# Kernel tuning notes

Measured on AMD Instinct MI355X. Metric: run time of the kernel, lower is better.

The kernel has to match this reference:

```python
import jax, jax.numpy as jnp
import numpy as np

BS = 8            # self.b from __init__
NSAMPLE = 32      # self.nsample
EPS_TCR = 0.2     # TotalCodingRate eps
COS_EPS = 1e-8    # torch cosine_similarity eps


def setup_inputs() -> dict:
    key = jax.random.key(0)
    k0, k1, k2, k3, k4 = jax.random.split(key, 5)
    B, N, C = 8, 8192, 64
    return {
        "logits": jax.random.normal(k0, (B, N, C), jnp.float32),
        "logits1": jax.random.normal(k1, (B, N, C), jnp.float32),
        "p0first": jax.random.uniform(k2, (B, N, 3), jnp.float32),
        "p0sec": jax.random.uniform(k3, (B, N, 3), jnp.float32),
        "orixyz": jax.random.uniform(k4, (B, N, 3), jnp.float32),
    }


def _fps(p, m):
    # furthest point sampling, seed = point 0; p: [b,n,3] -> idx [b,m] int32
    b, n, _ = p.shape
    batch = jnp.arange(b)
    d0 = jnp.sum((p - p[:, :1]) ** 2, -1)  # [b,n] sq dist to seed

    def step(dist, _):
        nxt = jnp.argmax(dist, axis=1)                 # [b]
        pn = p[batch, nxt]                             # [b,3]
        dist = jnp.minimum(dist, jnp.sum((p - pn[:, None]) ** 2, -1))
        return dist, nxt

    _, idxs = jax.lax.scan(step, d0, None, length=m - 1)  # [m-1,b]
    return jnp.concatenate(
        [jnp.zeros((b, 1), jnp.int32), idxs.T.astype(jnp.int32)], axis=1)


def _knn_idx(q, s, k):
    # q: [b,m,3] queries, s: [b,n,3] support -> [b,m,k] neighbor indices
    d = (jnp.sum(q * q, -1)[:, :, None] + jnp.sum(s * s, -1)[:, None, :]
         - 2.0 * jnp.einsum('bmd,bnd->bmn', q, s))
    _, idx = jax.lax.top_k(-d, k)  # smallest distances
    return idx


def _group_losses(fi, fj, c):
    # fi: [b,m,c] center feats, fj: [b,m,k,c] neighbor feats
    # per group: datatemp = cat(fj, fi) -> [K=k+1, c]
    D = jnp.concatenate([fj, fi[:, :, None, :]], axis=2)  # [b,m,K,c]
    avg = D.mean(axis=2, keepdims=True)                   # [b,m,1,c]
    num = jnp.sum(D * avg, -1)                            # [b,m,K]
    den = jnp.maximum(
        jnp.linalg.norm(D, axis=-1) * jnp.linalg.norm(avg, axis=-1), COS_EPS)
    loss_contract = -(num / den).mean(axis=2)             # [b,m] (Similarity_Loss)
    # TotalCodingRate on each single row z: -0.5*logdet(I + (c/(BS*eps)) z z^T)
    #   = -0.5*log(1 + (c/(BS*eps)) ||z||^2)   (rank-1 identity)
    scalar = c / (BS * EPS_TCR)
    loss_tcr = (-0.5 * jnp.log1p(scalar * jnp.sum(D * D, -1))).mean(axis=2)
    return jnp.sum(200.0 * loss_contract + 1.0 * loss_tcr, axis=1)  # [b]


def reference(logits, logits1, p0first, p0sec, orixyz):
    b, n, c = logits.shape
    ds = n // 16  # downsample

    # global per-point cosine loss
    num = jnp.sum(logits * logits1, -1)
    den = jnp.maximum(
        jnp.linalg.norm(logits, axis=-1) * jnp.linalg.norm(logits1, axis=-1),
        COS_EPS)
    globalpointloss = -jnp.mean(num / den)

    idx = _fps(p0first, ds)   # [b,ds]
    idx1 = _fps(p0sec, ds)
    new_p = jnp.take_along_axis(p0first, idx[..., None], axis=1)   # [b,ds,3]
    new_p1 = jnp.take_along_axis(p0sec, idx1[..., None], axis=1)
    fi = jnp.take_along_axis(logits, idx[..., None], axis=1)       # [b,ds,c]
    fi1 = jnp.take_along_axis(logits1, idx1[..., None], axis=1)

    ki = _knn_idx(new_p, p0first, NSAMPLE)    # [b,ds,k]
    ki1 = _knn_idx(new_p1, p0sec, NSAMPLE)
    fj = jax.vmap(lambda f, i: f[i])(logits, ki)    # [b,ds,k,c]
    fj1 = jax.vmap(lambda f, i: f[i])(logits1, ki1)

    # per-batch summed group-inner losses (both views)
    S = _group_losses(fi, fj, c) + _group_losses(fi1, fj1, c)  # [b]

    # faithful to original: running total divided by downsample each batch iter
    def fold(g, s):
        return (g + s) / ds, None
    groupinnerloss, _ = jax.lax.scan(fold, jnp.float32(0.0), S)
    groupinnerloss = groupinnerloss / b

    # original returns globalpointloss + groupinnerloss + groupinnerloss
    # (groupouterloss is computed but never used in the returned loss)
    return globalpointloss + groupinnerloss + groupinnerloss
```

## Files before the change

kernel.cpp:

```cpp
#include <hip/hip_runtime.h>
#include <cstdint>

#define NPTS 8192
#define NB 8
#define DS 512
#define CF 64
#define KNN 32
#define NFPS 16
#define NWORK 240
#define NCOSI 64
#define NITEMS (NCOSI + 2 * NB * DS)
#define DYNLDS 98304

typedef float v2f __attribute__((ext_vector_type(2)));
typedef unsigned long long ull;

__device__ __forceinline__ float wave_max63(float x) {
  int v;
  v = __builtin_amdgcn_update_dpp(0, __float_as_int(x), 0x111, 0xf, 0xf, true); x = fmaxf(x, __int_as_float(v));
  v = __builtin_amdgcn_update_dpp(0, __float_as_int(x), 0x112, 0xf, 0xf, true); x = fmaxf(x, __int_as_float(v));
  v = __builtin_amdgcn_update_dpp(0, __float_as_int(x), 0x114, 0xf, 0xf, true); x = fmaxf(x, __int_as_float(v));
  v = __builtin_amdgcn_update_dpp(0, __float_as_int(x), 0x118, 0xf, 0xf, true); x = fmaxf(x, __int_as_float(v));
  v = __builtin_amdgcn_update_dpp(0, __float_as_int(x), 0x142, 0xf, 0xf, true); x = fmaxf(x, __int_as_float(v));
  v = __builtin_amdgcn_update_dpp(0, __float_as_int(x), 0x143, 0xf, 0xf, true); x = fmaxf(x, __int_as_float(v));
  return x;
}

__device__ __forceinline__ float wave_sum_bcast(float x) {
  int v;
  v = __builtin_amdgcn_update_dpp(0, __float_as_int(x), 0x111, 0xf, 0xf, true); x += __int_as_float(v);
  v = __builtin_amdgcn_update_dpp(0, __float_as_int(x), 0x112, 0xf, 0xf, true); x += __int_as_float(v);
  v = __builtin_amdgcn_update_dpp(0, __float_as_int(x), 0x114, 0xf, 0xf, true); x += __int_as_float(v);
  v = __builtin_amdgcn_update_dpp(0, __float_as_int(x), 0x118, 0xf, 0xf, true); x += __int_as_float(v);
  v = __builtin_amdgcn_update_dpp(0, __float_as_int(x), 0x142, 0xf, 0xf, true); x += __int_as_float(v);
  v = __builtin_amdgcn_update_dpp(0, __float_as_int(x), 0x143, 0xf, 0xf, true); x += __int_as_float(v);
  return __int_as_float(__builtin_amdgcn_readlane(__float_as_int(x), 63));
}

__global__ __launch_bounds__(64) void zero_kernel(float* __restrict__ acc) {
  if (threadIdx.x < 16) acc[threadIdx.x] = 0.0f;
}

__global__ __launch_bounds__(512, 2) void fused_kernel(
    const float* __restrict__ logits, const float* __restrict__ logits1,
    const float* __restrict__ p0first, const float* __restrict__ p0sec,
    int* __restrict__ idxbuf, float* __restrict__ acc,
    int* __restrict__ done, float* __restrict__ out) {
  extern __shared__ char smem[];
  __shared__ __align__(16) ull wslot[2][8];
  __shared__ int wtot[8];
  __shared__ int s_bl[2];
  __shared__ int ctr, eqctr, s_center;
  __shared__ float wloss[8];

  const int blk = blockIdx.x;
  const int t = threadIdx.x;

  if (blk < NFPS) {
    float* ldsP = (float*)smem;
    const int view = blk >> 3, b = blk & 7;
    const float* p = (view ? p0sec : p0first) + (size_t)b * NPTS * 3;
    int* idx_out = idxbuf + blk * DS;
    const int lane = t & 63, wave = t >> 6;
    v2f px2[8], py2[8], pz2[8], dist2[8];
    {
      float f48[48];
      const float4* p4 = (const float4*)p;
      float4* l4 = (float4*)ldsP;
#pragma unroll
      for (int i = 0; i < 12; ++i) {
        float4 v4 = p4[t * 12 + i];
        l4[t * 12 + i] = v4;
        f48[i * 4 + 0] = v4.x; f48[i * 4 + 1] = v4.y;
        f48[i * 4 + 2] = v4.z; f48[i * 4 + 3] = v4.w;
      }
#pragma unroll
      for (int g = 0; g < 8; ++g) {
        px2[g] = (v2f){f48[6 * g + 0], f48[6 * g + 3]};
        py2[g] = (v2f){f48[6 * g + 1], f48[6 * g + 4]};
        pz2[g] = (v2f){f48[6 * g + 2], f48[6 * g + 5]};
        dist2[g] = (v2f){3.4e38f, 3.4e38f};
      }
    }
#pragma unroll
    for (int g = 0; g < 8; ++g) {
      asm("" : "+v"(px2[g]), "+v"(py2[g]), "+v"(pz2[g]));
    }
    if (t == 0)
      __hip_atomic_store(&idx_out[0], 0, __ATOMIC_RELAXED, __HIP_MEMORY_SCOPE_AGENT);
    float wx = p[0], wy = p[1], wz = p[2];
    __syncthreads();

    for (int it = 0; it < DS - 1; ++it) {
      v2f wx2 = (v2f){wx, wx}, wy2 = (v2f){wy, wy}, wz2 = (v2f){wz, wz};
#pragma unroll
      for (int g = 0; g < 8; ++g) {
        v2f dx = px2[g] - wx2, dy = py2[g] - wy2, dz = pz2[g] - wz2;
        v2f nd = dx * dx + dy * dy + dz * dz;
        dist2[g] = __builtin_elementwise_min(dist2[g], nd);
      }
      v2f m0 = __builtin_elementwise_max(dist2[0], dist2[1]);
      v2f m1 = __builtin_elementwise_max(dist2[2], dist2[3]);
      v2f m2 = __builtin_elementwise_max(dist2[4], dist2[5]);
      v2f m3 = __builtin_elementwise_max(dist2[6], dist2[7]);
      v2f n0 = __builtin_elementwise_max(m0, m1);
      v2f n1 = __builtin_elementwise_max(m2, m3);
      v2f q = __builtin_elementwise_max(n0, n1);
      float lm = fmaxf(q.x, q.y);
      float wmv = wave_max63(lm);
      float wm = __int_as_float(__builtin_amdgcn_readlane(__float_as_int(wmv), 63));
      ull cmask = __ballot(lm == wm);
      int winlane = (int)__ffsll(cmask) - 1;
      if (lane == winlane) {
        int jbest = 0;
#pragma unroll
        for (int jp = 15; jp >= 0; --jp) {
          float dv = (jp & 1) ? dist2[jp >> 1].y : dist2[jp >> 1].x;
          if (dv == lm) jbest = jp;
        }
        unsigned e_best = ((unsigned)t << 4) | (unsigned)jbest;
        wslot[it & 1][wave] =
            (((ull)__float_as_uint(wm)) << 32) | (ull)(8191u - e_best);
      }
      asm volatile("s_waitcnt lgkmcnt(0)\n\ts_barrier" ::: "memory");
      {
        const ull* ws = wslot[it & 1];
        ull k0 = ws[0], k1 = ws[1], k2 = ws[2], k3 = ws[3];
        ull k4 = ws[4], k5 = ws[5], k6 = ws[6], k7 = ws[7];
        ull a0 = k0 > k1 ? k0 : k1, a1 = k2 > k3 ? k2 : k3;
        ull a2 = k4 > k5 ? k4 : k5, a3 = k6 > k7 ? k6 : k7;
        ull b0 = a0 > a1 ? a0 : a1, b1 = a2 > a3 ? a2 : a3;
        ull kb = b0 > b1 ? b0 : b1;
        unsigned e = 8191u - (unsigned)(kb & 0xffffffffu);
        if (t == 0)
          __hip_atomic_store(&idx_out[it + 1], (int)e, __ATOMIC_RELAXED,
                             __HIP_MEMORY_SCOPE_AGENT);
        wx = ldsP[e * 3 + 0]; wy = ldsP[e * 3 + 1]; wz = ldsP[e * 3 + 2];
      }
    }
  } else {
    int* hb0 = (int*)smem;
    int* hb1 = (int*)(smem + 16384);
    float* Drows = (float*)(smem + 32768);
    int* nbr = (int*)(smem + 41216);
    int* eq = (int*)(smem + 41344);
    const int lane = t & 63, wave = t >> 6;
    const int w0 = blk - NFPS;
    for (int item = w0; item < NITEMS; item += NWORK) {
      if (item < NCOSI) {
        float cv = 0.0f;
#pragma unroll
        for (int rr = 0; rr < 2; ++rr) {
          int row = item * 1024 + rr * 512 + t;
          const float4* A = (const float4*)(logits + (size_t)row * CF);
          const float4* Bv = (const float4*)(logits1 + (size_t)row * CF);
          float ab = 0.f, aa = 0.f, bb = 0.f;
#pragma unroll
          for (int i = 0; i < 16; ++i) {
            float4 a = A[i], c4 = Bv[i];
            ab += a.x * c4.x + a.y * c4.y + a.z * c4.z + a.w * c4.w;
            aa += a.x * a.x + a.y * a.y + a.z * a.z + a.w * a.w;
            bb += c4.x * c4.x + c4.y * c4.y + c4.z * c4.z + c4.w * c4.w;
          }
          cv += ab / fmaxf(sqrtf(aa) * sqrtf(bb), 1e-8f);
        }
        cv = wave_sum_bcast(cv);
        if (lane == 0) wloss[wave] = cv;
        __syncthreads();
        if (t == 0) {
          float s = 0.f;
#pragma unroll
          for (int w = 0; w < 8; ++w) s += wloss[w];
          atomicAdd(&acc[0], s);
        }
        __syncthreads();
      } else {
        const int qi2 = item - NCOSI;
        const int m = qi2 >> 4, pair = qi2 & 15;
        const int g = pair * DS + m;
        const int view = pair >> 3, b = pair & 7;
        const float* p = (view ? p0sec : p0first) + (size_t)b * NPTS * 3;
        float f48[48];
        {
          const float4* p4 = (const float4*)p;
#pragma unroll
          for (int i = 0; i < 12; ++i) {
            float4 v4 = p4[t * 12 + i];
            f48[i * 4 + 0] = v4.x; f48[i * 4 + 1] = v4.y;
            f48[i * 4 + 2] = v4.z; f48[i * 4 + 3] = v4.w;
          }
        }
        for (int k = t; k < 4096; k += 512) hb0[k] = 0;
        if (t == 0) {
          int ce;
          while ((unsigned)(ce = __hip_atomic_load(&idxbuf[g], __ATOMIC_RELAXED,
                                                   __HIP_MEMORY_SCOPE_AGENT)) >= 8192u)
            __builtin_amdgcn_s_sleep(2);
          s_center = ce;
        }
        __syncthreads();
        const int ci = s_center;
        const float qx = p[ci * 3], qy = p[ci * 3 + 1], qz = p[ci * 3 + 2];
        const float qq = qx * qx + qy * qy + qz * qz;
        const int cpy = (t & 1) << 11;
        unsigned sk[16];
#pragma unroll
        for (int j = 0; j < 16; ++j) {
          float sx = f48[j * 3], sy = f48[j * 3 + 1], sz = f48[j * 3 + 2];
          float ss = sx * sx + sy * sy + sz * sz;
          float dt = qx * sx + qy * sy + qz * sz;
          float d = qq + ss - 2.0f * dt;
          unsigned u = __float_as_uint(d);
          u = (u & 0x80000000u) ? ~u : (u | 0x80000000u);
          sk[j] = u;
        }
        int rrank = 31;
#pragma unroll
        for (int j = 0; j < 16; ++j) atomicAdd(&hb0[cpy + (sk[j] >> 21)], 1);
        __syncthreads();
        unsigned pA, pAB, V;
        {
          int b0 = t << 2;
          int c0 = hb0[b0] + hb0[2048 + b0];
          int c1 = hb0[b0 + 1] + hb0[2048 + b0 + 1];
          int c2 = hb0[b0 + 2] + hb0[2048 + b0 + 2];
          int c3 = hb0[b0 + 3] + hb0[2048 + b0 + 3];
          int s = c0 + c1 + c2 + c3;
          int inc = s;
#pragma unroll
          for (int o = 1; o < 64; o <<= 1) {
            int v = __shfl_up(inc, o, 64);
            if (lane >= o) inc += v;
          }
          if (lane == 63) wtot[wave] = inc;
          for (int k = t; k < 4096; k += 512) hb1[k] = 0;
          __syncthreads();
          int off = 0;
#pragma unroll
          for (int w = 0; w < 8; ++w) off += (w < wave) ? wtot[w] : 0;
          int exc = off + inc - s;
          if (rrank >= exc && rrank < exc + s) {
            int r2 = rrank - exc; int bin, less;
            if (r2 < c0) { bin = 0; less = 0; }
            else if (r2 < c0 + c1) { bin = 1; less = c0; }
            else if (r2 < c0 + c1 + c2) { bin = 2; less = c0 + c1; }
            else { bin = 3; less = c0 + c1 + c2; }
            s_bl[0] = b0 + bin; s_bl[1] = exc + less;
          }
          __syncthreads();
          pA = (unsigned)s_bl[0];
          rrank -= s_bl[1];
        }
#pragma unroll
        for (int j = 0; j < 16; ++j) {
          unsigned u = sk[j];
          if ((u >> 21) == pA) atomicAdd(&hb1[cpy + ((u >> 10) & 2047)], 1);
        }
        __syncthreads();
        {
          int b0 = t << 2;
          int c0 = hb1[b0] + hb1[2048 + b0];
          int c1 = hb1[b0 + 1] + hb1[2048 + b0 + 1];
          int c2 = hb1[b0 + 2] + hb1[2048 + b0 + 2];
          int c3 = hb1[b0 + 3] + hb1[2048 + b0 + 3];
          int s = c0 + c1 + c2 + c3;
          int inc = s;
#pragma unroll
          for (int o = 1; o < 64; o <<= 1) {
            int v = __shfl_up(inc, o, 64);
            if (lane >= o) inc += v;
          }
          if (lane == 63) wtot[wave] = inc;
          for (int k = t; k < 4096; k += 512) hb0[k] = 0;
          __syncthreads();
          int off = 0;
#pragma unroll
          for (int w = 0; w < 8; ++w) off += (w < wave) ? wtot[w] : 0;
          int exc = off + inc - s;
          if (rrank >= exc && rrank < exc + s) {
            int r2 = rrank - exc; int bin, less;
            if (r2 < c0) { bin = 0; less = 0; }
            else if (r2 < c0 + c1) { bin = 1; less = c0; }
            else if (r2 < c0 + c1 + c2) { bin = 2; less = c0 + c1; }
            else { bin = 3; less = c0 + c1 + c2; }
            s_bl[0] = b0 + bin; s_bl[1] = exc + less;
          }
          __syncthreads();
          pAB = (pA << 11) | (unsigned)s_bl[0];
          rrank -= s_bl[1];
        }
        const int cpyC = (t & 1) << 10;
#pragma unroll
        for (int j = 0; j < 16; ++j) {
          unsigned u = sk[j];
          if ((u >> 10) == pAB) atomicAdd(&hb0[cpyC + (u & 1023)], 1);
        }
        __syncthreads();
        {
          int b0 = t << 1;
          int c0 = hb0[b0] + hb0[1024 + b0];
          int c1 = hb0[b0 + 1] + hb0[1024 + b0 + 1];
          int s = c0 + c1;
          int inc = s;
#pragma unroll
          for (int o = 1; o < 64; o <<= 1) {
            int v = __shfl_up(inc, o, 64);
            if (lane >= o) inc += v;
          }
          if (lane == 63) wtot[wave] = inc;
          __syncthreads();
          int off = 0;
#pragma unroll
          for (int w = 0; w < 8; ++w) off += (w < wave) ? wtot[w] : 0;
          int exc = off + inc - s;
          if (rrank >= exc && rrank < exc + s) {
            int r2 = rrank - exc;
            if (r2 < c0) { s_bl[0] = b0; s_bl[1] = exc; }
            else { s_bl[0] = b0 + 1; s_bl[1] = exc + c0; }
          }
          if (t == 0) { ctr = 0; eqctr = 0; }
          __syncthreads();
          V = (pAB << 10) | (unsigned)s_bl[0];
          rrank -= s_bl[1];
        }
#pragma unroll
        for (int j = 0; j < 16; ++j) {
          unsigned u = sk[j];
          if (u < V) {
            int s = atomicAdd(&ctr, 1);
            nbr[s] = t * 16 + j;
          } else if (u == V) {
            int s2 = atomicAdd(&eqctr, 1);
            if (s2 < 256) eq[s2] = t * 16 + j;
          }
        }
        __syncthreads();
        if (t == 0) {
          int need = rrank + 1;
          int E = eqctr; if (E > 256) E = 256;
          int base = KNN - need;
          for (int s = 0; s < need; ++s) {
            int mi = 0;
            for (int i = 1; i < E; ++i)
              if (eq[i] < eq[mi]) mi = i;
            nbr[base + s] = eq[mi];
            eq[mi] = 0x7fffffff;
          }
        }
        __syncthreads();
        const float* f = (view ? logits1 : logits) + (size_t)b * NPTS * CF;
        for (int r = wave; r < 33; r += 8) {
          int e = (r < 32) ? nbr[r] : ci;
          Drows[r * 64 + lane] = f[(size_t)e * CF + lane];
        }
        __syncthreads();
        float avg = 0.0f;
#pragma unroll
        for (int r = 0; r < 33; ++r) avg += Drows[r * 64 + lane];
        avg *= (1.0f / 33.0f);
        float na = wave_sum_bcast(avg * avg);
        const float rsna = sqrtf(na);
        float loss = 0.0f;
        for (int r = wave; r < 33; r += 8) {
          float d = Drows[r * 64 + lane];
          float d0 = wave_sum_bcast(d * avg);
          float n0 = wave_sum_bcast(d * d);
          float den = fmaxf(sqrtf(n0) * rsna, 1e-8f);
          loss += -200.0f * (d0 / den) - 0.5f * log1pf(40.0f * n0);
        }
        if (lane == 0) wloss[wave] = loss;
        __syncthreads();
        if (t == 0) {
          float s = 0.f;
#pragma unroll
          for (int w = 0; w < 8; ++w) s += wloss[w];
          atomicAdd(&acc[1 + b], s * (1.0f / 33.0f));
        }
        __syncthreads();
      }
    }
    __syncthreads();
    if (t == 0) {
      int d = __hip_atomic_fetch_add(done, 1, __ATOMIC_ACQ_REL, __HIP_MEMORY_SCOPE_AGENT);
      if (d == NWORK - 1) {
        float a0 = __hip_atomic_load(&acc[0], __ATOMIC_ACQUIRE, __HIP_MEMORY_SCOPE_AGENT);
        float gsum = 0.0f;
        for (int bb = 0; bb < 8; ++bb) {
          float Sb = __hip_atomic_load(&acc[1 + bb], __ATOMIC_ACQUIRE, __HIP_MEMORY_SCOPE_AGENT);
          gsum = (gsum + Sb) * (1.0f / 512.0f);
        }
        gsum *= 0.125f;
        out[0] = -a0 / 65536.0f + gsum + gsum;
      }
    }
  }
}

extern "C" void kernel_launch(void* const* d_in, const int* in_sizes, int n_in,
                              void* d_out, int out_size, void* d_ws, size_t ws_size,
                              hipStream_t stream) {
  (void)in_sizes; (void)n_in; (void)out_size; (void)ws_size;
  const float* logits  = (const float*)d_in[0];
  const float* logits1 = (const float*)d_in[1];
  const float* p0first = (const float*)d_in[2];
  const float* p0sec   = (const float*)d_in[3];
  float* out = (float*)d_out;

  float* acc = (float*)d_ws;
  int* done  = (int*)d_ws + 13;
  int* idxbuf = (int*)d_ws + 16;

  zero_kernel<<<1, 64, 0, stream>>>(acc);
  fused_kernel<<<NFPS + NWORK, 512, DYNLDS, stream>>>(logits, logits1, p0first, p0sec,
                                                      idxbuf, acc, done, out);
}
```

Before: 524.6 us.

## Run two FPS instances per block to interleave independent reduction chains

Each FPS block now processes two point clouds at once, so there are 8 FPS blocks instead of 16 and more blocks go to the worker pool. The two independent distance-update and wave-max chains are interleaved to hide DPP and barrier latency and to halve the number of barriers per pair of clouds. The winner's coordinates are now fetched from global memory (L1/L2) instead of an LDS copy, which adds global-load latency on the serial critical path of every iteration. Register pressure also doubles in the FPS path.

```diff
diff --git a/kernel.cpp b/kernel.cpp
--- a/kernel.cpp
+++ b/kernel.cpp
@@ -6,8 +6,8 @@
 #define DS 512
 #define CF 64
 #define KNN 32
-#define NFPS 16
-#define NWORK 240
+#define NFPS 8
+#define NWORK 248
 #define NCOSI 64
 #define NITEMS (NCOSI + 2 * NB * DS)
 #define DYNLDS 98304
@@ -15,15 +15,14 @@
 typedef float v2f __attribute__((ext_vector_type(2)));
 typedef unsigned long long ull;
 
-__device__ __forceinline__ float wave_max63(float x) {
-  int v;
-  v = __builtin_amdgcn_update_dpp(0, __float_as_int(x), 0x111, 0xf, 0xf, true); x = fmaxf(x, __int_as_float(v));
-  v = __builtin_amdgcn_update_dpp(0, __float_as_int(x), 0x112, 0xf, 0xf, true); x = fmaxf(x, __int_as_float(v));
-  v = __builtin_amdgcn_update_dpp(0, __float_as_int(x), 0x114, 0xf, 0xf, true); x = fmaxf(x, __int_as_float(v));
-  v = __builtin_amdgcn_update_dpp(0, __float_as_int(x), 0x118, 0xf, 0xf, true); x = fmaxf(x, __int_as_float(v));
-  v = __builtin_amdgcn_update_dpp(0, __float_as_int(x), 0x142, 0xf, 0xf, true); x = fmaxf(x, __int_as_float(v));
-  v = __builtin_amdgcn_update_dpp(0, __float_as_int(x), 0x143, 0xf, 0xf, true); x = fmaxf(x, __int_as_float(v));
-  return x;
+__device__ __forceinline__ void wave_max63_dual(float& a, float& b) {
+  int va, vb;
+#define DSTEP(ctrl)                                                            \
+  va = __builtin_amdgcn_update_dpp(0, __float_as_int(a), ctrl, 0xf, 0xf, true);\
+  vb = __builtin_amdgcn_update_dpp(0, __float_as_int(b), ctrl, 0xf, 0xf, true);\
+  a = fmaxf(a, __int_as_float(va)); b = fmaxf(b, __int_as_float(vb));
+  DSTEP(0x111) DSTEP(0x112) DSTEP(0x114) DSTEP(0x118) DSTEP(0x142) DSTEP(0x143)
+#undef DSTEP
 }
 
 __device__ __forceinline__ float wave_sum_bcast(float x) {
@@ -47,7 +46,8 @@
     int* __restrict__ idxbuf, float* __restrict__ acc,
     int* __restrict__ done, float* __restrict__ out) {
   extern __shared__ char smem[];
-  __shared__ __align__(16) ull wslot[2][8];
+  __shared__ __align__(16) ull wslotA[2][8];
+  __shared__ __align__(16) ull wslotB[2][8];
   __shared__ int wtot[8];
   __shared__ int s_bl[2];
   __shared__ int ctr, eqctr, s_center;
@@ -57,85 +57,144 @@
   const int t = threadIdx.x;
 
   if (blk < NFPS) {
-    float* ldsP = (float*)smem;
-    const int view = blk >> 3, b = blk & 7;
-    const float* p = (view ? p0sec : p0first) + (size_t)b * NPTS * 3;
-    int* idx_out = idxbuf + blk * DS;
+    const int iA = blk * 2, iB = blk * 2 + 1;
+    const float* pA = ((iA >> 3) ? p0sec : p0first) + (size_t)(iA & 7) * NPTS * 3;
+    const float* pB = ((iB >> 3) ? p0sec : p0first) + (size_t)(iB & 7) * NPTS * 3;
+    int* idxA = idxbuf + iA * DS;
+    int* idxB = idxbuf + iB * DS;
     const int lane = t & 63, wave = t >> 6;
-    v2f px2[8], py2[8], pz2[8], dist2[8];
+
+    v2f pxA[8], pyA[8], pzA[8], dA[8];
+    v2f pxB[8], pyB[8], pzB[8], dB[8];
     {
-      float f48[48];
-      const float4* p4 = (const float4*)p;
-      float4* l4 = (float4*)ldsP;
-#pragma unroll
-      for (int i = 0; i < 12; ++i) {
-        float4 v4 = p4[t * 12 + i];
-        l4[t * 12 + i] = v4;
-        f48[i * 4 + 0] = v4.x; f48[i * 4 + 1] = v4.y;
-        f48[i * 4 + 2] = v4.z; f48[i * 4 + 3] = v4.w;
-      }
+      const float4* a4 = (const float4*)pA;
+      const float4* b4 = (const float4*)pB;
+#pragma unroll
+      for (int k = 0; k < 4; ++k) {
+        float4 v0 = a4[t * 12 + 3 * k + 0];
+        float4 v1 = a4[t * 12 + 3 * k + 1];
+        float4 v2 = a4[t * 12 + 3 * k + 2];
+        pxA[2 * k]     = (v2f){v0.x, v0.w};
+        pyA[2 * k]     = (v2f){v0.y, v1.x};
+        pzA[2 * k]     = (v2f){v0.z, v1.y};
+        pxA[2 * k + 1] = (v2f){v1.z, v2.y};
+        pyA[2 * k + 1] = (v2f){v1.w, v2.z};
+        pzA[2 * k + 1] = (v2f){v2.x, v2.w};
+        dA[2 * k] = (v2f){3.4e38f, 3.4e38f};
+        dA[2 * k + 1] = (v2f){3.4e38f, 3.4e38f};
+        float4 u0 = b4[t * 12 + 3 * k + 0];
+        float4 u1 = b4[t * 12 + 3 * k + 1];
+        float4 u2 = b4[t * 12 + 3 * k + 2];
+        pxB[2 * k]     = (v2f){u0.x, u0.w};
+        pyB[2 * k]     = (v2f){u0.y, u1.x};
+        pzB[2 * k]     = (v2f){u0.z, u1.y};
+        pxB[2 * k + 1] = (v2f){u1.z, u2.y};
+        pyB[2 * k + 1] = (v2f){u1.w, u2.z};
+        pzB[2 * k + 1] = (v2f){u2.x, u2.w};
+        dB[2 * k] = (v2f){3.4e38f, 3.4e38f};
+        dB[2 * k + 1] = (v2f){3.4e38f, 3.4e38f};
+      }
+    }
+#pragma unroll
+    for (int g = 0; g < 8; ++g) {
+      asm("" : "+v"(pxA[g]), "+v"(pyA[g]), "+v"(pzA[g]));
+      asm("" : "+v"(pxB[g]), "+v"(pyB[g]), "+v"(pzB[g]));
+    }
+    if (t == 0) {
+      __hip_atomic_store(&idxA[0], 0, __ATOMIC_RELAXED, __HIP_MEMORY_SCOPE_AGENT);
+      __hip_atomic_store(&idxB[0], 0, __ATOMIC_RELAXED, __HIP_MEMORY_SCOPE_AGENT);
+    }
+    float wxA = pA[0], wyA = pA[1], wzA = pA[2];
+    float wxB = pB[0], wyB = pB[1], wzB = pB[2];
+
+    for (int it = 0; it < DS - 1; ++it) {
+      v2f ax = (v2f){wxA, wxA}, ay = (v2f){wyA, wyA}, az = (v2f){wzA, wzA};
+      v2f bx = (v2f){wxB, wxB}, by = (v2f){wyB, wyB}, bz = (v2f){wzB, wzB};
 #pragma unroll
       for (int g = 0; g < 8; ++g) {
-        px2[g] = (v2f){f48[6 * g + 0], f48[6 * g + 3]};
-        py2[g] = (v2f){f48[6 * g + 1], f48[6 * g + 4]};
-        pz2[g] = (v2f){f48[6 * g + 2], f48[6 * g + 5]};
-        dist2[g] = (v2f){3.4e38f, 3.4e38f};
-      }
-    }
-#pragma unroll
-    for (int g = 0; g < 8; ++g) {
-      asm("" : "+v"(px2[g]), "+v"(py2[g]), "+v"(pz2[g]));
-    }
-    if (t == 0)
-      __hip_atomic_store(&idx_out[0], 0, __ATOMIC_RELAXED, __HIP_MEMORY_SCOPE_AGENT);
-    float wx = p[0], wy = p[1], wz = p[2];
-    __syncthreads();
-
-    for (int it = 0; it < DS - 1; ++it) {
-      v2f wx2 = (v2f){wx, wx}, wy2 = (v2f){wy, wy}, wz2 = (v2f){wz, wz};
-#pragma unroll
-      for (int g = 0; g < 8; ++g) {
-        v2f dx = px2[g] - wx2, dy = py2[g] - wy2, dz = pz2[g] - wz2;
-        v2f nd = dx * dx + dy * dy + dz * dz;
-        dist2[g] = __builtin_elementwise_min(dist2[g], nd);
-      }
-      v2f m0 = __builtin_elementwise_max(dist2[0], dist2[1]);
-      v2f m1 = __builtin_elementwise_max(dist2[2], dist2[3]);
-      v2f m2 = __builtin_elementwise_max(dist2[4], dist2[5]);
-      v2f m3 = __builtin_elementwise_max(dist2[6], dist2[7]);
-      v2f n0 = __builtin_elementwise_max(m0, m1);
-      v2f n1 = __builtin_elementwise_max(m2, m3);
-      v2f q = __builtin_elementwise_max(n0, n1);
-      float lm = fmaxf(q.x, q.y);
-      float wmv = wave_max63(lm);
-      float wm = __int_as_float(__builtin_amdgcn_readlane(__float_as_int(wmv), 63));
-      ull cmask = __ballot(lm == wm);
-      int winlane = (int)__ffsll(cmask) - 1;
-      if (lane == winlane) {
-        int jbest = 0;
+        v2f dxa = pxA[g] - ax, dya = pyA[g] - ay, dza = pzA[g] - az;
+        v2f nda = dxa * dxa + dya * dya + dza * dza;
+        dA[g] = __builtin_elementwise_min(dA[g], nda);
+        v2f dxb = pxB[g] - bx, dyb = pyB[g] - by, dzb = pzB[g] - bz;
+        v2f ndb = dxb * dxb + dyb * dyb + dzb * dzb;
+        dB[g] = __builtin_elementwise_min(dB[g], ndb);
+      }
+      v2f a0 = __builtin_elementwise_max(dA[0], dA[1]);
+      v2f a1 = __builtin_elementwise_max(dA[2], dA[3]);
+      v2f a2 = __builtin_elementwise_max(dA[4], dA[5]);
+      v2f a3 = __builtin_elementwise_max(dA[6], dA[7]);
+      v2f b0 = __builtin_elementwise_max(dB[0], dB[1]);
+      v2f b1 = __builtin_elementwise_max(dB[2], dB[3]);
+      v2f b2 = __builtin_elementwise_max(dB[4], dB[5]);
+      v2f b3 = __builtin_elementwise_max(dB[6], dB[7]);
+      v2f a4 = __builtin_elementwise_max(a0, a1);
+      v2f a5 = __builtin_elementwise_max(a2, a3);
+      v2f b4 = __builtin_elementwise_max(b0, b1);
+      v2f b5 = __builtin_elementwise_max(b2, b3);
+      v2f a6 = __builtin_elementwise_max(a4, a5);
+      v2f b6 = __builtin_elementwise_max(b4, b5);
+      float lmA = fmaxf(a6.x, a6.y);
+      float lmB = fmaxf(b6.x, b6.y);
+      float rA = lmA, rB = lmB;
+      wave_max63_dual(rA, rB);
+      float wmA = __int_as_float(__builtin_amdgcn_readlane(__float_as_int(rA), 63));
+      float wmB = __int_as_float(__builtin_amdgcn_readlane(__float_as_int(rB), 63));
+      ull cmA = __ballot(lmA == wmA);
+      ull cmB = __ballot(lmB == wmB);
+      int wlA = (int)__ffsll(cmA) - 1;
+      int wlB = (int)__ffsll(cmB) - 1;
+      if (lane == wlA) {
+        int jb = 0;
 #pragma unroll
         for (int jp = 15; jp >= 0; --jp) {
-          float dv = (jp & 1) ? dist2[jp >> 1].y : dist2[jp >> 1].x;
-          if (dv == lm) jbest = jp;
-        }
-        unsigned e_best = ((unsigned)t << 4) | (unsigned)jbest;
-        wslot[it & 1][wave] =
-            (((ull)__float_as_uint(wm)) << 32) | (ull)(8191u - e_best);
+          float dv = (jp & 1) ? dA[jp >> 1].y : dA[jp >> 1].x;
+          if (dv == lmA) jb = jp;
+        }
+        unsigned e_best = ((unsigned)t << 4) | (unsigned)jb;
+        wslotA[it & 1][wave] =
+            (((ull)__float_as_uint(wmA)) << 32) | (ull)(8191u - e_best);
+      }
+      if (lane == wlB) {
+        int jb = 0;
+#pragma unroll
+        for (int jp = 15; jp >= 0; --jp) {
+          float dv = (jp & 1) ? dB[jp >> 1].y : dB[jp >> 1].x;
+          if (dv == lmB) jb = jp;
+        }
+        unsigned e_best = ((unsigned)t << 4) | (unsigned)jb;
+        wslotB[it & 1][wave] =
+            (((ull)__float_as_uint(wmB)) << 32) | (ull)(8191u - e_best);
       }
       asm volatile("s_waitcnt lgkmcnt(0)\n\ts_barrier" ::: "memory");
       {
-        const ull* ws = wslot[it & 1];
-        ull k0 = ws[0], k1 = ws[1], k2 = ws[2], k3 = ws[3];
-        ull k4 = ws[4], k5 = ws[5], k6 = ws[6], k7 = ws[7];
-        ull a0 = k0 > k1 ? k0 : k1, a1 = k2 > k3 ? k2 : k3;
-        ull a2 = k4 > k5 ? k4 : k5, a3 = k6 > k7 ? k6 : k7;
-        ull b0 = a0 > a1 ? a0 : a1, b1 = a2 > a3 ? a2 : a3;
-        ull kb = b0 > b1 ? b0 : b1;
-        unsigned e = 8191u - (unsigned)(kb & 0xffffffffu);
-        if (t == 0)
-          __hip_atomic_store(&idx_out[it + 1], (int)e, __ATOMIC_RELAXED,
+        const ull* wsA = wslotA[it & 1];
+        const ull* wsB = wslotB[it & 1];
+        ull kA0 = wsA[0], kA1 = wsA[1], kA2 = wsA[2], kA3 = wsA[3];
+        ull kA4 = wsA[4], kA5 = wsA[5], kA6 = wsA[6], kA7 = wsA[7];
+        ull kB0 = wsB[0], kB1 = wsB[1], kB2 = wsB[2], kB3 = wsB[3];
+        ull kB4 = wsB[4], kB5 = wsB[5], kB6 = wsB[6], kB7 = wsB[7];
+        ull qa0 = kA0 > kA1 ? kA0 : kA1, qa1 = kA2 > kA3 ? kA2 : kA3;
+        ull qa2 = kA4 > kA5 ? kA4 : kA5, qa3 = kA6 > kA7 ? kA6 : kA7;
+        ull qb0 = kB0 > kB1 ? kB0 : kB1, qb1 = kB2 > kB3 ? kB2 : kB3;
+        ull qb2 = kB4 > kB5 ? kB4 : kB5, qb3 = kB6 > kB7 ? kB6 : kB7;
+        ull ra0 = qa0 > qa1 ? qa0 : qa1, ra1 = qa2 > qa3 ? qa2 : qa3;
+        ull rb0 = qb0 > qb1 ? qb0 : qb1, rb1 = qb2 > qb3 ? qb2 : qb3;
+        ull kfA = ra0 > ra1 ? ra0 : ra1;
+        ull kfB = rb0 > rb1 ? rb0 : rb1;
+        unsigned eA = 8191u - (unsigned)(kfA & 0xffffffffu);
+        unsigned eB = 8191u - (unsigned)(kfB & 0xffffffffu);
+        if (t == 0) {
+          __hip_atomic_store(&idxA[it + 1], (int)eA, __ATOMIC_RELAXED,
                              __HIP_MEMORY_SCOPE_AGENT);
-        wx = ldsP[e * 3 + 0]; wy = ldsP[e * 3 + 1]; wz = ldsP[e * 3 + 2];
+          __hip_atomic_store(&idxB[it + 1], (int)eB, __ATOMIC_RELAXED,
+                             __HIP_MEMORY_SCOPE_AGENT);
+        }
+        const float* cA = pA + (size_t)eA * 3;
+        const float* cB = pB + (size_t)eB * 3;
+        float nAx = cA[0], nAy = cA[1], nAz = cA[2];
+        float nBx = cB[0], nBy = cB[1], nBz = cB[2];
+        wxA = nAx; wyA = nAy; wzA = nAz;
+        wxB = nBx; wyB = nBy; wzB = nBz;
       }
     }
   } else {
```

After: 1.153 ms. +119.7%, slower.
